# Performance work log

Hardware: AMD Instinct MI355X
Metric: run time of the kernel (lower is better)

Reference implementation:

```python
import jax, jax.numpy as jnp
import numpy as np

K = 4096   # infeatures
N = 11008  # outfeatures
T = 8192   # tokens (batch*seq)
GROUP = 32
E8M0_BIAS = 127
E2M1_VALS = jnp.array([0.0, 0.5, 1.0, 1.5, 2.0, 3.0, 4.0, 6.0], dtype=jnp.float32)


def setup_inputs() -> dict:
    key = jax.random.key(0)
    k1, k2, k3, k4 = jax.random.split(key, 4)
    x = jax.random.normal(k1, (T, K), dtype=jnp.float32)
    # packed fp4: 8 nibbles per int32 along the in-feature axis -> [K//8, N]
    weight_packed = jax.random.randint(k2, (K // 8, N), 0, 2147483647, dtype=jnp.int32)
    # e8m0 exponents near the bias so 2^(e-127) stays well-conditioned in fp32
    weight_scale_e8m0 = 112 + jax.random.randint(k3, (K // GROUP, N), 0, 30, dtype=jnp.int32)
    bias = jax.random.normal(k4, (N,), dtype=jnp.float32)
    return {"x": x, "weight_packed": weight_packed,
            "weight_scale_e8m0": weight_scale_e8m0, "bias": bias}


def dequantize_weight(weight_packed, weight_scale_e8m0):
    # unpack 8 fp4 nibbles per int32: nibble j -> in-feature row r*8 + j
    shifts = (jnp.arange(8, dtype=jnp.int32) * 4)[None, :, None]       # [1,8,1]
    nib = (weight_packed[:, None, :] >> shifts) & 0xF                   # [K//8,8,N]
    mag = E2M1_VALS[nib & 0x7]                                           # e2m1 magnitude
    sign = jnp.where((nib >> 3) & 1 == 1, -1.0, 1.0).astype(jnp.float32)
    w = (mag * sign).reshape(K, N)
    # per-group e8m0 scale: 2^(e - 127), groups of 32 along in-features
    scale = jnp.exp2((weight_scale_e8m0 - E8M0_BIAS).astype(jnp.float32))  # [K//32,N]
    w = (w.reshape(K // GROUP, GROUP, N) * scale[:, None, :]).reshape(K, N)
    return w


def reference(x, weight_packed, weight_scale_e8m0, bias):
    w = dequantize_weight(weight_packed, weight_scale_e8m0)  # [K, N]
    return x @ w + bias                                       # [T, N]
```

## Files before the change

### kernel.cpp

```cpp
#include <hip/hip_runtime.h>


#define TDIM 8192
#define KDIM 4096
#define NDIM 11008

typedef __attribute__((ext_vector_type(8))) short short8;
typedef __attribute__((ext_vector_type(8))) unsigned short ushort8;
typedef __attribute__((ext_vector_type(4))) float f32x4;

__device__ __forceinline__ unsigned short f2bf(float f) {
    unsigned int u = __float_as_uint(f);
    u += 0x7FFFu + ((u >> 16) & 1u);
    return (unsigned short)(u >> 16);
}

__device__ __forceinline__ unsigned short nib2bf(unsigned int v, int e) {
    unsigned int m3 = v & 7u;
    if (m3 == 0u) return 0;
    unsigned int s = (v & 8u) << 12;
    unsigned int E = (unsigned int)e + (m3 >> 1) - 1u;
    unsigned int man = (m3 >= 2u) ? ((m3 & 1u) << 6) : 0u;
    return (unsigned short)(s | (E << 7) | man);
}

__device__ __forceinline__ void gload_lds16(const void* g, void* l) {
    __builtin_amdgcn_global_load_lds(
        (const __attribute__((address_space(1))) void*)g,
        (__attribute__((address_space(3))) void*)l, 16, 0, 0);
}

__global__ __launch_bounds__(256) void convert_x(const float* __restrict__ x,
                                                 unsigned short* __restrict__ xbf) {
    size_t i = ((size_t)blockIdx.x * 256 + threadIdx.x) * 8;
    float4 v0 = *(const float4*)(x + i);
    float4 v1 = *(const float4*)(x + i + 4);
    ushort8 r;
    r[0] = f2bf(v0.x); r[1] = f2bf(v0.y); r[2] = f2bf(v0.z); r[3] = f2bf(v0.w);
    r[4] = f2bf(v1.x); r[5] = f2bf(v1.y); r[6] = f2bf(v1.z); r[7] = f2bf(v1.w);
    *(ushort8*)(xbf + i) = r;
}

__global__ __launch_bounds__(256) void dequant_w(const int* __restrict__ wp,
                                                 const int* __restrict__ wse,
                                                 unsigned short* __restrict__ wt) {
    __shared__ int sT[64][65];
    const int tid = threadIdx.x;
    const int n0 = blockIdx.x * 64;
    const int r0 = blockIdx.y * 64;

    #pragma unroll
    for (int i = 0; i < 16; ++i) {
        int idx = i * 256 + tid;
        int r = idx >> 6, n = idx & 63;
        sT[r][n] = wp[(size_t)(r0 + r) * NDIM + n0 + n];
    }
    __syncthreads();
    #pragma unroll
    for (int i = 0; i < 16; ++i) {
        int idx = i * 256 + tid;
        int n = idx >> 6, r = idx & 63;
        unsigned int p = (unsigned int)sT[r][n];
        int e = wse[(size_t)((r0 + r) >> 2) * NDIM + n0 + n];
        ushort8 o;
        #pragma unroll
        for (int j = 0; j < 8; ++j) o[j] = nib2bf((p >> (4 * j)) & 0xFu, e);
        *(ushort8*)(wt + (size_t)(n0 + n) * KDIM + (size_t)(r0 + r) * 8) = o;
    }
}

#define STG(PJ0, PJ1, GOFF, C, MAT, HK)                                        \
    do {                                                                       \
        gload_lds16((PJ0) + (GOFF), ldsW + (C)*32768 + (MAT)*16384 + (HK)*8192);           \
        gload_lds16((PJ1) + (GOFF), ldsW + (C)*32768 + (MAT)*16384 + (HK)*8192 + 4096);    \
    } while (0)

#define RD_A(CB, KS, MH, DST)                                                                  \
    DST[0] = *(const short8*)(ldsC + (CB)*65536 + (KS)*16384 + ((MH)*4 + 0)*1024 + aoff);      \
    DST[1] = *(const short8*)(ldsC + (CB)*65536 + (KS)*16384 + ((MH)*4 + 1)*1024 + aoff);      \
    DST[2] = *(const short8*)(ldsC + (CB)*65536 + (KS)*16384 + ((MH)*4 + 2)*1024 + aoff);      \
    DST[3] = *(const short8*)(ldsC + (CB)*65536 + (KS)*16384 + ((MH)*4 + 3)*1024 + aoff);

#define RD_B(CB, KS, DST)                                                                      \
    DST[0] = *(const short8*)(ldsC + (CB)*65536 + 32768 + (KS)*16384 + 0*1024 + boff);         \
    DST[1] = *(const short8*)(ldsC + (CB)*65536 + 32768 + (KS)*16384 + 1*1024 + boff);         \
    DST[2] = *(const short8*)(ldsC + (CB)*65536 + 32768 + (KS)*16384 + 2*1024 + boff);         \
    DST[3] = *(const short8*)(ldsC + (CB)*65536 + 32768 + (KS)*16384 + 3*1024 + boff);

#define CLUSTER(A, B, MH)                                                      \
    __builtin_amdgcn_s_setprio(1);                                             \
    _Pragma("unroll")                                                          \
    for (int i_ = 0; i_ < 4; ++i_) {                                           \
        _Pragma("unroll")                                                      \
        for (int n_ = 0; n_ < 4; ++n_)                                         \
            acc[(MH)*4 + i_][n_] = __builtin_amdgcn_mfma_f32_16x16x32_bf16(    \
                A[i_], B[n_], acc[(MH)*4 + i_][n_], 0, 0, 0);                  \
    }                                                                          \
    __builtin_amdgcn_s_setprio(0);

#define BODY(T, C)                                                             \
    do {                                                                       \
                       \
        if ((T) < 63) STG(pA0, pA1, 96, (C)^1, 0, 1);                          \
        RD_A((C), 0, 1, aY)                                                    \
        CLUSTER(aX, bX, 0)                                                     \
                \
        if ((T) < 63) STG(pB0, pB1, 96, (C)^1, 1, 1);                          \
        RD_B((C), 1, bY)                                                       \
        RD_A((C), 1, 0, aX)                                                    \
        CLUSTER(aY, bX, 1)                                                     \
        \
        if ((T) < 63) asm volatile("s_waitcnt vmcnt(4)" ::: "memory");         \
        __builtin_amdgcn_s_barrier();                                          \
               \
        if ((T) < 62) STG(pA0, pA1, 128, (C), 0, 0);                           \
        RD_A((C), 1, 1, aY)                                                    \
        CLUSTER(aX, bY, 0)                                                     \
                       \
        if ((T) < 62) STG(pB0, pB1, 128, (C), 1, 0);                           \
        if ((T) < 63) { RD_B((C)^1, 0, bX) RD_A((C)^1, 0, 0, aX) }             \
        CLUSTER(aY, bY, 1)                                                     \
            \
        if ((T) < 62)       asm volatile("s_waitcnt vmcnt(4)" ::: "memory");   \
        else if ((T) == 62) asm volatile("s_waitcnt vmcnt(0)" ::: "memory");   \
        __builtin_amdgcn_s_barrier();                                          \
        pA0 += 64; pA1 += 64; pB0 += 64; pB1 += 64;                            \
    } while (0)

__global__ __launch_bounds__(512, 1) void gemm256(const unsigned short* __restrict__ xbf,
                                                  const unsigned short* __restrict__ wt,
                                                  const float* __restrict__ bias,
                                                  float* __restrict__ out) {
    __shared__ __attribute__((aligned(16))) unsigned short lds[2][2][16384];
    const int tid = threadIdx.x;
    const int l = tid & 63, wid = tid >> 6;
    const int wm = wid >> 2, wn = wid & 3;

    int b = blockIdx.x;
    int swz = (b & 7) * 172 + (b >> 3);
    int band = swz / 344;
    int r = swz % 344;
    int st = r >> 5; if (st > 10) st = 10;
    int ii = r - (st << 5);
    int w = (st < 10) ? 4 : 3;
    const int bm0 = (band * 8 + ii / w) * 256;
    const int bn0 = (st * 4 + ii % w) * 256;

    int rs0, ks0, rs1, ks1;
    {
        int chunk = wid * 64 + l;
        int cin = chunk & 63;
        cin ^= ((cin >> 5) & 1) << 1;
        rs0 = (chunk >> 6) * 16 + (cin >> 2);
        ks0 = (cin & 3) * 8;
        chunk = 512 + wid * 64 + l;
        cin = chunk & 63;
        cin ^= ((cin >> 5) & 1) << 1;
        rs1 = (chunk >> 6) * 16 + (cin >> 2);
        ks1 = (cin & 3) * 8;
    }

    const unsigned short* pA0 = xbf + (size_t)(bm0 + rs0) * KDIM + ks0;
    const unsigned short* pA1 = xbf + (size_t)(bm0 + rs1) * KDIM + ks1;
    const unsigned short* pB0 = wt + (size_t)(bn0 + rs0) * KDIM + ks0;
    const unsigned short* pB1 = wt + (size_t)(bn0 + rs1) * KDIM + ks1;

    unsigned short* ldsW = &lds[0][0][0] + wid * 512;
    const char* ldsC = (const char*)&lds[0][0][0];

    const int lbyte = (((l & 15) * 64 + ((l >> 4) << 4))) ^ ((l & 8) << 2);
    const int aoff = wm * 8192 + lbyte;
    const int boff = wn * 4096 + lbyte;

    f32x4 acc[8][4] = {};
    short8 aX[4], aY[4], bX[4], bY[4];

    STG(pA0, pA1, 0, 0, 0, 0);
    STG(pB0, pB1, 0, 0, 1, 0);
    STG(pA0, pA1, 32, 0, 0, 1);
    STG(pB0, pB1, 32, 0, 1, 1);
    STG(pA0, pA1, 64, 1, 0, 0);
    STG(pB0, pB1, 64, 1, 1, 0);
    asm volatile("s_waitcnt vmcnt(4)" ::: "memory");
    __builtin_amdgcn_s_barrier();
    RD_B(0, 0, bX)
    RD_A(0, 0, 0, aX)

    for (int tt = 0; tt < 32; ++tt) {
        const int ta = 2 * tt;
        BODY(ta, 0);
        BODY(ta + 1, 1);
    }

    const int crow = (l >> 4) * 4, ccol = l & 15;
    #pragma unroll
    for (int nf = 0; nf < 4; ++nf) {
        int col = bn0 + wn * 64 + nf * 16 + ccol;
        float bv = bias[col];
        #pragma unroll
        for (int m = 0; m < 8; ++m) {
            int row0 = bm0 + wm * 128 + m * 16 + crow;
            #pragma unroll
            for (int j2 = 0; j2 < 4; ++j2)
                __builtin_nontemporal_store(acc[m][nf][j2] + bv,
                                            &out[(size_t)(row0 + j2) * NDIM + col]);
        }
    }
}

__global__ __launch_bounds__(256, 2) void gemm_fused(const float* __restrict__ x,
                                                     const int* __restrict__ wp,
                                                     const int* __restrict__ wse,
                                                     const float* __restrict__ bias,
                                                     float* __restrict__ out) {
    __shared__ __attribute__((aligned(16))) unsigned short lA[128 * 64];
    __shared__ __attribute__((aligned(16))) unsigned short lB[128 * 64];
    const int tid = threadIdx.x;
    const int l = tid & 63, wid = tid >> 6;
    const int bn0 = blockIdx.x * 128, bm0 = blockIdx.y * 128;
    const int wm = wid >> 1, wn = wid & 1;

    f32x4 acc[4][4] = {};

    for (int k0 = 0; k0 < KDIM; k0 += 64) {
        float4 av0[4], av1[4];
        unsigned int bp[4];
        int be[4];
        #pragma unroll
        for (int i = 0; i < 4; ++i) {
            int seg = i * 256 + tid;
            int row = seg >> 3, kseg = seg & 7;
            const float4* p = (const float4*)(x + (size_t)(bm0 + row) * KDIM + k0 + kseg * 8);
            av0[i] = p[0]; av1[i] = p[1];
        }
        #pragma unroll
        for (int i = 0; i < 4; ++i) {
            int idx = i * 256 + tid;
            int ln = idx & 127, lr = idx >> 7;
            bp[i] = ((const unsigned int*)wp)[(size_t)(k0 / 8 + lr) * NDIM + bn0 + ln];
            be[i] = wse[(size_t)((k0 + lr * 8) >> 5) * NDIM + bn0 + ln];
        }
        #pragma unroll
        for (int i = 0; i < 4; ++i) {
            int seg = i * 256 + tid;
            int row = seg >> 3, kseg = seg & 7;
            ushort8 r;
            r[0] = f2bf(av0[i].x); r[1] = f2bf(av0[i].y); r[2] = f2bf(av0[i].z); r[3] = f2bf(av0[i].w);
            r[4] = f2bf(av1[i].x); r[5] = f2bf(av1[i].y); r[6] = f2bf(av1[i].z); r[7] = f2bf(av1[i].w);
            *(ushort8*)&lA[row * 64 + kseg * 8] = r;
        }
        #pragma unroll
        for (int i = 0; i < 4; ++i) {
            int idx = i * 256 + tid;
            int ln = idx & 127, lr = idx >> 7;
            unsigned int p = bp[i];
            int e = be[i];
            ushort8 r;
            #pragma unroll
            for (int j = 0; j < 8; ++j) r[j] = nib2bf((p >> (4 * j)) & 0xFu, e);
            *(ushort8*)&lB[ln * 64 + lr * 8] = r;
        }
        __syncthreads();
        #pragma unroll
        for (int kc = 0; kc < 2; ++kc) {
            short8 a[4], bb[4];
            #pragma unroll
            for (int f = 0; f < 4; ++f) {
                a[f] = *(const short8*)&lA[(wm * 64 + f * 16 + (l & 15)) * 64 + kc * 32 + (l >> 4) * 8];
                bb[f] = *(const short8*)&lB[(wn * 64 + f * 16 + (l & 15)) * 64 + kc * 32 + (l >> 4) * 8];
            }
            #pragma unroll
            for (int fm = 0; fm < 4; ++fm)
                #pragma unroll
                for (int fn = 0; fn < 4; ++fn)
                    acc[fm][fn] = __builtin_amdgcn_mfma_f32_16x16x32_bf16(a[fm], bb[fn], acc[fm][fn], 0, 0, 0);
        }
        __syncthreads();
    }

    const int crow = (l >> 4) * 4, ccol = l & 15;
    #pragma unroll
    for (int fn = 0; fn < 4; ++fn) {
        int col = bn0 + wn * 64 + fn * 16 + ccol;
        float bv = bias[col];
        #pragma unroll
        for (int fm = 0; fm < 4; ++fm) {
            int row0 = bm0 + wm * 64 + fm * 16 + crow;
            #pragma unroll
            for (int j = 0; j < 4; ++j)
                out[(size_t)(row0 + j) * NDIM + col] = acc[fm][fn][j] + bv;
        }
    }
}

extern "C" void kernel_launch(void* const* d_in, const int* in_sizes, int n_in,
                              void* d_out, int out_size, void* d_ws, size_t ws_size,
                              hipStream_t stream) {
    (void)in_sizes; (void)n_in; (void)out_size;
    const float* x = (const float*)d_in[0];
    const int* wp = (const int*)d_in[1];
    const int* wse = (const int*)d_in[2];
    const float* bias = (const float*)d_in[3];
    float* out = (float*)d_out;

    const size_t xbf_bytes = (size_t)TDIM * KDIM * 2;
    const size_t wt_bytes = (size_t)NDIM * KDIM * 2;

    if (ws_size >= xbf_bytes + wt_bytes) {
        unsigned short* xbf = (unsigned short*)d_ws;
        unsigned short* wt = (unsigned short*)((char*)d_ws + xbf_bytes);
        hipLaunchKernelGGL(convert_x, dim3((TDIM * KDIM) / (256 * 8)), dim3(256), 0, stream, x, xbf);
        hipLaunchKernelGGL(dequant_w, dim3(NDIM / 64, (KDIM / 8) / 64), dim3(256), 0, stream, wp, wse, wt);
        hipLaunchKernelGGL(gemm256, dim3((NDIM / 256) * (TDIM / 256)), dim3(512), 0, stream, xbf, wt, bias, out);
    } else {
        hipLaunchKernelGGL(gemm_fused, dim3(NDIM / 128, TDIM / 128), dim3(256), 0, stream, x, wp, wse, bias, out);
    }
}
```

Before: 688.1 us.

## Switch main GEMM from 16x16x32 to 32x32x16 bf16 MFMA tiles

Replaces the 16x16x32 bf16 MFMA instructions in the 256-tile GEMM with 32x32x16 MFMAs. The LDS fragment read offsets, the accumulator layout (f32x16 [4][2]) and the epilogue row/column mapping are reworked to match. Larger MFMA tiles cut the instruction count and give more operand reuse per LDS read, but they change the bank access pattern of the swizzled LDS reads and have a longer per-instruction latency.

```diff
diff --git a/kernel.cpp b/kernel.cpp
--- a/kernel.cpp
+++ b/kernel.cpp
@@ -8,6 +8,7 @@
 typedef __attribute__((ext_vector_type(8))) short short8;
 typedef __attribute__((ext_vector_type(8))) unsigned short ushort8;
 typedef __attribute__((ext_vector_type(4))) float f32x4;
+typedef __attribute__((ext_vector_type(16))) float f32x16;
 
 __device__ __forceinline__ unsigned short f2bf(float f) {
     unsigned int u = __float_as_uint(f);
@@ -75,26 +76,29 @@
         gload_lds16((PJ1) + (GOFF), ldsW + (C)*32768 + (MAT)*16384 + (HK)*8192 + 4096);    \
     } while (0)
 
-#define RD_A(CB, KS, MH, DST)                                                                  \
-    DST[0] = *(const short8*)(ldsC + (CB)*65536 + (KS)*16384 + ((MH)*4 + 0)*1024 + aoff);      \
-    DST[1] = *(const short8*)(ldsC + (CB)*65536 + (KS)*16384 + ((MH)*4 + 1)*1024 + aoff);      \
-    DST[2] = *(const short8*)(ldsC + (CB)*65536 + (KS)*16384 + ((MH)*4 + 2)*1024 + aoff);      \
-    DST[3] = *(const short8*)(ldsC + (CB)*65536 + (KS)*16384 + ((MH)*4 + 3)*1024 + aoff);
-
-#define RD_B(CB, KS, DST)                                                                      \
-    DST[0] = *(const short8*)(ldsC + (CB)*65536 + 32768 + (KS)*16384 + 0*1024 + boff);         \
-    DST[1] = *(const short8*)(ldsC + (CB)*65536 + 32768 + (KS)*16384 + 1*1024 + boff);         \
-    DST[2] = *(const short8*)(ldsC + (CB)*65536 + 32768 + (KS)*16384 + 2*1024 + boff);         \
-    DST[3] = *(const short8*)(ldsC + (CB)*65536 + 32768 + (KS)*16384 + 3*1024 + boff);
-
-#define CLUSTER(A, B, MH)                                                      \
+#define RD_A32(CB, KS, MH, DST)                                                                \
+    DST[0] = *(const short8*)(ldsC + (CB)*65536 + (KS)*16384 + (((MH)*2+0)*2)*1024 + aoff + ofK0); \
+    DST[1] = *(const short8*)(ldsC + (CB)*65536 + (KS)*16384 + (((MH)*2+0)*2)*1024 + aoff + ofK1); \
+    DST[2] = *(const short8*)(ldsC + (CB)*65536 + (KS)*16384 + (((MH)*2+1)*2)*1024 + aoff + ofK0); \
+    DST[3] = *(const short8*)(ldsC + (CB)*65536 + (KS)*16384 + (((MH)*2+1)*2)*1024 + aoff + ofK1);
+
+#define RD_B32(CB, KS, DST)                                                                    \
+    DST[0] = *(const short8*)(ldsC + (CB)*65536 + 32768 + (KS)*16384 + 0*2048 + boff + ofK0);  \
+    DST[1] = *(const short8*)(ldsC + (CB)*65536 + 32768 + (KS)*16384 + 0*2048 + boff + ofK1);  \
+    DST[2] = *(const short8*)(ldsC + (CB)*65536 + 32768 + (KS)*16384 + 1*2048 + boff + ofK0);  \
+    DST[3] = *(const short8*)(ldsC + (CB)*65536 + 32768 + (KS)*16384 + 1*2048 + boff + ofK1);
+
+#define CLUSTER32(A, B, MH)                                                    \
     __builtin_amdgcn_s_setprio(1);                                             \
     _Pragma("unroll")                                                          \
-    for (int i_ = 0; i_ < 4; ++i_) {                                           \
+    for (int kk_ = 0; kk_ < 2; ++kk_) {                                        \
         _Pragma("unroll")                                                      \
-        for (int n_ = 0; n_ < 4; ++n_)                                         \
-            acc[(MH)*4 + i_][n_] = __builtin_amdgcn_mfma_f32_16x16x32_bf16(    \
-                A[i_], B[n_], acc[(MH)*4 + i_][n_], 0, 0, 0);                  \
+        for (int m_ = 0; m_ < 2; ++m_) {                                       \
+            _Pragma("unroll")                                                  \
+            for (int n_ = 0; n_ < 2; ++n_)                                     \
+                acc[(MH)*2 + m_][n_] = __builtin_amdgcn_mfma_f32_32x32x16_bf16( \
+                    A[m_*2 + kk_], B[n_*2 + kk_], acc[(MH)*2 + m_][n_], 0, 0, 0); \
+        }                                                                      \
     }                                                                          \
     __builtin_amdgcn_s_setprio(0);
 
@@ -102,25 +106,23 @@
     do {                                                                       \
                        \
         if ((T) < 63) STG(pA0, pA1, 96, (C)^1, 0, 1);                          \
-        RD_A((C), 0, 1, aY)                                                    \
-        CLUSTER(aX, bX, 0)                                                     \
+        RD_A32((C), 0, 1, aY)                                                  \
+        CLUSTER32(aX, bX, 0)                                                   \
                 \
         if ((T) < 63) STG(pB0, pB1, 96, (C)^1, 1, 1);                          \
-        RD_B((C), 1, bY)                                                       \
-        RD_A((C), 1, 0, aX)                                                    \
-        CLUSTER(aY, bX, 1)                                                     \
-        \
+        RD_B32((C), 1, bY)                                                     \
+        RD_A32((C), 1, 0, aX)                                                  \
+        CLUSTER32(aY, bX, 1)                                                   \
         if ((T) < 63) asm volatile("s_waitcnt vmcnt(4)" ::: "memory");         \
         __builtin_amdgcn_s_barrier();                                          \
-               \
+              \
         if ((T) < 62) STG(pA0, pA1, 128, (C), 0, 0);                           \
-        RD_A((C), 1, 1, aY)                                                    \
-        CLUSTER(aX, bY, 0)                                                     \
+        RD_A32((C), 1, 1, aY)                                                  \
+        CLUSTER32(aX, bY, 0)                                                   \
                        \
         if ((T) < 62) STG(pB0, pB1, 128, (C), 1, 0);                           \
-        if ((T) < 63) { RD_B((C)^1, 0, bX) RD_A((C)^1, 0, 0, aX) }             \
-        CLUSTER(aY, bY, 1)                                                     \
-            \
+        if ((T) < 63) { RD_B32((C)^1, 0, bX) RD_A32((C)^1, 0, 0, aX) }         \
+        CLUSTER32(aY, bY, 1)                                                   \
         if ((T) < 62)       asm volatile("s_waitcnt vmcnt(4)" ::: "memory");   \
         else if ((T) == 62) asm volatile("s_waitcnt vmcnt(0)" ::: "memory");   \
         __builtin_amdgcn_s_barrier();                                          \
@@ -168,11 +170,14 @@
     unsigned short* ldsW = &lds[0][0][0] + wid * 512;
     const char* ldsC = (const char*)&lds[0][0][0];
 
-    const int lbyte = (((l & 15) * 64 + ((l >> 4) << 4))) ^ ((l & 8) << 2);
-    const int aoff = wm * 8192 + lbyte;
-    const int boff = wn * 4096 + lbyte;
-
-    f32x4 acc[8][4] = {};
+    const int s3 = (l >> 3) & 1;
+    const int lbase = ((l >> 4) & 1) * 1024 + (l & 15) * 64 + ((l >> 5) << 4);
+    const int ofK0 = lbase + (s3 << 5);
+    const int ofK1 = lbase + ((s3 ^ 1) << 5);
+    const int aoff = wm * 8192;
+    const int boff = wn * 4096;
+
+    f32x16 acc[4][2] = {};
     short8 aX[4], aY[4], bX[4], bY[4];
 
     STG(pA0, pA1, 0, 0, 0, 0);
@@ -183,27 +188,28 @@
     STG(pB0, pB1, 64, 1, 1, 0);
     asm volatile("s_waitcnt vmcnt(4)" ::: "memory");
     __builtin_amdgcn_s_barrier();
-    RD_B(0, 0, bX)
-    RD_A(0, 0, 0, aX)
+    RD_B32(0, 0, bX)
+    RD_A32(0, 0, 0, aX)
 
     for (int tt = 0; tt < 32; ++tt) {
-        const int ta = 2 * tt;
-        BODY(ta, 0);
-        BODY(ta + 1, 1);
-    }
-
-    const int crow = (l >> 4) * 4, ccol = l & 15;
+        BODY(2 * tt, 0);
+        BODY(2 * tt + 1, 1);
+    }
+
+    const int ecol = l & 31, erow = (l >> 5) * 4;
     #pragma unroll
-    for (int nf = 0; nf < 4; ++nf) {
-        int col = bn0 + wn * 64 + nf * 16 + ccol;
+    for (int nb = 0; nb < 2; ++nb) {
+        int col = bn0 + wn * 64 + nb * 32 + ecol;
         float bv = bias[col];
         #pragma unroll
-        for (int m = 0; m < 8; ++m) {
-            int row0 = bm0 + wm * 128 + m * 16 + crow;
-            #pragma unroll
-            for (int j2 = 0; j2 < 4; ++j2)
-                __builtin_nontemporal_store(acc[m][nf][j2] + bv,
-                                            &out[(size_t)(row0 + j2) * NDIM + col]);
+        for (int mb = 0; mb < 4; ++mb) {
+            int rowbase = bm0 + wm * 128 + mb * 32 + erow;
+            #pragma unroll
+            for (int reg = 0; reg < 16; ++reg) {
+                int row = rowbase + (reg & 3) + 8 * (reg >> 2);
+                __builtin_nontemporal_store(acc[mb][nb][reg] + bv,
+                                            &out[(size_t)row * NDIM + col]);
+            }
         }
     }
 }
```

Result: slower. 734.8 us (+6.8%).

## Merge prepass kernels and split GEMM tail into 256x128 tiles

Applied to the files above, without the earlier changes.

Fuses the x-to-bf16 conversion and the weight dequant into one prepass launch to save a kernel launch and the gap between them. The GEMM is split in two launches: 1280 full 256x256 tiles, then the last 96 tiles processed as 192 half-width 256x128 tiles via a templated NF=2 variant. The split is meant to balance the final wave across CUs, since 1376 tiles do not divide evenly over the compute units. In exchange it adds an extra launch, and the half-width tiles have lower arithmetic intensity.

```diff
diff --git a/kernel.cpp b/kernel.cpp
--- a/kernel.cpp
+++ b/kernel.cpp
@@ -30,24 +30,26 @@
         (__attribute__((address_space(3))) void*)l, 16, 0, 0);
 }
 
-__global__ __launch_bounds__(256) void convert_x(const float* __restrict__ x,
-                                                 unsigned short* __restrict__ xbf) {
-    size_t i = ((size_t)blockIdx.x * 256 + threadIdx.x) * 8;
-    float4 v0 = *(const float4*)(x + i);
-    float4 v1 = *(const float4*)(x + i + 4);
-    ushort8 r;
-    r[0] = f2bf(v0.x); r[1] = f2bf(v0.y); r[2] = f2bf(v0.z); r[3] = f2bf(v0.w);
-    r[4] = f2bf(v1.x); r[5] = f2bf(v1.y); r[6] = f2bf(v1.z); r[7] = f2bf(v1.w);
-    *(ushort8*)(xbf + i) = r;
-}
-
-__global__ __launch_bounds__(256) void dequant_w(const int* __restrict__ wp,
-                                                 const int* __restrict__ wse,
-                                                 unsigned short* __restrict__ wt) {
+__global__ __launch_bounds__(256) void prepass(const float* __restrict__ x,
+                                               unsigned short* __restrict__ xbf,
+                                               const int* __restrict__ wp,
+                                               const int* __restrict__ wse,
+                                               unsigned short* __restrict__ wt) {
     __shared__ int sT[64][65];
     const int tid = threadIdx.x;
-    const int n0 = blockIdx.x * 64;
-    const int r0 = blockIdx.y * 64;
+    if (blockIdx.x < 16384) {
+        size_t i = ((size_t)blockIdx.x * 256 + tid) * 8;
+        float4 v0 = *(const float4*)(x + i);
+        float4 v1 = *(const float4*)(x + i + 4);
+        ushort8 r;
+        r[0] = f2bf(v0.x); r[1] = f2bf(v0.y); r[2] = f2bf(v0.z); r[3] = f2bf(v0.w);
+        r[4] = f2bf(v1.x); r[5] = f2bf(v1.y); r[6] = f2bf(v1.z); r[7] = f2bf(v1.w);
+        *(ushort8*)(xbf + i) = r;
+        return;
+    }
+    const int bb = blockIdx.x - 16384;
+    const int n0 = (bb % 172) * 64;
+    const int r0 = (bb / 172) * 64;
 
     #pragma unroll
     for (int i = 0; i < 16; ++i) {
@@ -69,64 +71,77 @@
     }
 }
 
-#define STG(PJ0, PJ1, GOFF, C, MAT, HK)                                        \
-    do {                                                                       \
-        gload_lds16((PJ0) + (GOFF), ldsW + (C)*32768 + (MAT)*16384 + (HK)*8192);           \
-        gload_lds16((PJ1) + (GOFF), ldsW + (C)*32768 + (MAT)*16384 + (HK)*8192 + 4096);    \
+#define STG_A(GOFF, C, HK)                                                                  \
+    do {                                                                                    \
+        gload_lds16(pA0 + (GOFF), ldsW + (C)*32768 + (HK)*8192);                            \
+        gload_lds16(pA1 + (GOFF), ldsW + (C)*32768 + (HK)*8192 + 4096);                     \
     } while (0)
 
-#define RD_A(CB, KS, MH, DST)                                                                  \
-    DST[0] = *(const short8*)(ldsC + (CB)*65536 + (KS)*16384 + ((MH)*4 + 0)*1024 + aoff);      \
-    DST[1] = *(const short8*)(ldsC + (CB)*65536 + (KS)*16384 + ((MH)*4 + 1)*1024 + aoff);      \
-    DST[2] = *(const short8*)(ldsC + (CB)*65536 + (KS)*16384 + ((MH)*4 + 2)*1024 + aoff);      \
+#define STG_B(GOFF, C, HK)                                                                  \
+    do {                                                                                    \
+        gload_lds16(pB0 + (GOFF), ldsW + (C)*32768 + 16384 + (HK)*8192);                    \
+        if constexpr (NF == 4)                                                              \
+            gload_lds16(pB1 + (GOFF), ldsW + (C)*32768 + 16384 + (HK)*8192 + 4096);         \
+    } while (0)
+
+#define RD_A(CB, KS, MH, DST)                                                                      \
+    DST[0] = *(const short8*)(ldsC + (CB)*65536 + (KS)*16384 + ((MH)*4 + 0)*1024 + aoff);          \
+    DST[1] = *(const short8*)(ldsC + (CB)*65536 + (KS)*16384 + ((MH)*4 + 1)*1024 + aoff);          \
+    DST[2] = *(const short8*)(ldsC + (CB)*65536 + (KS)*16384 + ((MH)*4 + 2)*1024 + aoff);          \
     DST[3] = *(const short8*)(ldsC + (CB)*65536 + (KS)*16384 + ((MH)*4 + 3)*1024 + aoff);
 
-#define RD_B(CB, KS, DST)                                                                      \
-    DST[0] = *(const short8*)(ldsC + (CB)*65536 + 32768 + (KS)*16384 + 0*1024 + boff);         \
-    DST[1] = *(const short8*)(ldsC + (CB)*65536 + 32768 + (KS)*16384 + 1*1024 + boff);         \
-    DST[2] = *(const short8*)(ldsC + (CB)*65536 + 32768 + (KS)*16384 + 2*1024 + boff);         \
-    DST[3] = *(const short8*)(ldsC + (CB)*65536 + 32768 + (KS)*16384 + 3*1024 + boff);
+#define RD_B(CB, KS, DST)                                                                          \
+    DST[0] = *(const short8*)(ldsC + (CB)*65536 + 32768 + (KS)*16384 + 0*1024 + boff);             \
+    DST[1] = *(const short8*)(ldsC + (CB)*65536 + 32768 + (KS)*16384 + 1*1024 + boff);             \
+    if constexpr (NF == 4) {                                                                       \
+        DST[2] = *(const short8*)(ldsC + (CB)*65536 + 32768 + (KS)*16384 + 2*1024 + boff);         \
+        DST[3] = *(const short8*)(ldsC + (CB)*65536 + 32768 + (KS)*16384 + 3*1024 + boff);         \
+    }
 
 #define CLUSTER(A, B, MH)                                                      \
     __builtin_amdgcn_s_setprio(1);                                             \
     _Pragma("unroll")                                                          \
     for (int i_ = 0; i_ < 4; ++i_) {                                           \
         _Pragma("unroll")                                                      \
-        for (int n_ = 0; n_ < 4; ++n_)                                         \
+        for (int n_ = 0; n_ < NF; ++n_)                                        \
             acc[(MH)*4 + i_][n_] = __builtin_amdgcn_mfma_f32_16x16x32_bf16(    \
                 A[i_], B[n_], acc[(MH)*4 + i_][n_], 0, 0, 0);                  \
     }                                                                          \
     __builtin_amdgcn_s_setprio(0);
 
+#define VWAIT_STEADY()                                                         \
+    do { if constexpr (NF == 4) asm volatile("s_waitcnt vmcnt(4)" ::: "memory"); \
+         else                   asm volatile("s_waitcnt vmcnt(3)" ::: "memory"); } while (0)
+
 #define BODY(T, C)                                                             \
     do {                                                                       \
                        \
-        if ((T) < 63) STG(pA0, pA1, 96, (C)^1, 0, 1);                          \
+        if ((T) < 63) STG_A(96, (C)^1, 1);                                     \
         RD_A((C), 0, 1, aY)                                                    \
         CLUSTER(aX, bX, 0)                                                     \
                 \
-        if ((T) < 63) STG(pB0, pB1, 96, (C)^1, 1, 1);                          \
+        if ((T) < 63) STG_B(96, (C)^1, 1);                                     \
         RD_B((C), 1, bY)                                                       \
         RD_A((C), 1, 0, aX)                                                    \
         CLUSTER(aY, bX, 1)                                                     \
-        \
-        if ((T) < 63) asm volatile("s_waitcnt vmcnt(4)" ::: "memory");         \
+             \
+        if ((T) < 63) VWAIT_STEADY();                                          \
         __builtin_amdgcn_s_barrier();                                          \
-               \
-        if ((T) < 62) STG(pA0, pA1, 128, (C), 0, 0);                           \
+              \
+        if ((T) < 62) STG_A(128, (C), 0);                                      \
         RD_A((C), 1, 1, aY)                                                    \
         CLUSTER(aX, bY, 0)                                                     \
                        \
-        if ((T) < 62) STG(pB0, pB1, 128, (C), 1, 0);                           \
+        if ((T) < 62) STG_B(128, (C), 0);                                      \
         if ((T) < 63) { RD_B((C)^1, 0, bX) RD_A((C)^1, 0, 0, aX) }             \
         CLUSTER(aY, bY, 1)                                                     \
-            \
-        if ((T) < 62)       asm volatile("s_waitcnt vmcnt(4)" ::: "memory");   \
+        if ((T) < 62)       VWAIT_STEADY();                                    \
         else if ((T) == 62) asm volatile("s_waitcnt vmcnt(0)" ::: "memory");   \
         __builtin_amdgcn_s_barrier();                                          \
         pA0 += 64; pA1 += 64; pB0 += 64; pB1 += 64;                            \
     } while (0)
 
+template<int NF>
 __global__ __launch_bounds__(512, 1) void gemm256(const unsigned short* __restrict__ xbf,
                                                   const unsigned short* __restrict__ wt,
                                                   const float* __restrict__ bias,
@@ -137,14 +152,21 @@
     const int wm = wid >> 2, wn = wid & 3;
 
     int b = blockIdx.x;
-    int swz = (b & 7) * 172 + (b >> 3);
+    int swz, half = 0;
+    if constexpr (NF == 4) {
+        swz = (b & 7) * 160 + (b >> 3);
+    } else {
+        int js = (b & 7) * 24 + (b >> 3);
+        swz = 1280 + (js >> 1);
+        half = js & 1;
+    }
     int band = swz / 344;
     int r = swz % 344;
     int st = r >> 5; if (st > 10) st = 10;
     int ii = r - (st << 5);
     int w = (st < 10) ? 4 : 3;
     const int bm0 = (band * 8 + ii / w) * 256;
-    const int bn0 = (st * 4 + ii % w) * 256;
+    const int bn0 = (st * 4 + ii % w) * 256 + half * 128;
 
     int rs0, ks0, rs1, ks1;
     {
@@ -170,32 +192,29 @@
 
     const int lbyte = (((l & 15) * 64 + ((l >> 4) << 4))) ^ ((l & 8) << 2);
     const int aoff = wm * 8192 + lbyte;
-    const int boff = wn * 4096 + lbyte;
+    const int boff = wn * (NF * 1024) + lbyte;
 
     f32x4 acc[8][4] = {};
     short8 aX[4], aY[4], bX[4], bY[4];
 
-    STG(pA0, pA1, 0, 0, 0, 0);
-    STG(pB0, pB1, 0, 0, 1, 0);
-    STG(pA0, pA1, 32, 0, 0, 1);
-    STG(pB0, pB1, 32, 0, 1, 1);
-    STG(pA0, pA1, 64, 1, 0, 0);
-    STG(pB0, pB1, 64, 1, 1, 0);
-    asm volatile("s_waitcnt vmcnt(4)" ::: "memory");
+    STG_A(0, 0, 0);   STG_B(0, 0, 0);
+    STG_A(32, 0, 1);  STG_B(32, 0, 1);
+    STG_A(64, 1, 0);  STG_B(64, 1, 0);
+    if constexpr (NF == 4) asm volatile("s_waitcnt vmcnt(4)" ::: "memory");
+    else                   asm volatile("s_waitcnt vmcnt(3)" ::: "memory");
     __builtin_amdgcn_s_barrier();
     RD_B(0, 0, bX)
     RD_A(0, 0, 0, aX)
 
     for (int tt = 0; tt < 32; ++tt) {
-        const int ta = 2 * tt;
-        BODY(ta, 0);
-        BODY(ta + 1, 1);
+        BODY(2 * tt, 0);
+        BODY(2 * tt + 1, 1);
     }
 
     const int crow = (l >> 4) * 4, ccol = l & 15;
     #pragma unroll
-    for (int nf = 0; nf < 4; ++nf) {
-        int col = bn0 + wn * 64 + nf * 16 + ccol;
+    for (int nf = 0; nf < NF; ++nf) {
+        int col = bn0 + wn * (NF * 16) + nf * 16 + ccol;
         float bv = bias[col];
         #pragma unroll
         for (int m = 0; m < 8; ++m) {
@@ -309,9 +328,9 @@
     if (ws_size >= xbf_bytes + wt_bytes) {
         unsigned short* xbf = (unsigned short*)d_ws;
         unsigned short* wt = (unsigned short*)((char*)d_ws + xbf_bytes);
-        hipLaunchKernelGGL(convert_x, dim3((TDIM * KDIM) / (256 * 8)), dim3(256), 0, stream, x, xbf);
-        hipLaunchKernelGGL(dequant_w, dim3(NDIM / 64, (KDIM / 8) / 64), dim3(256), 0, stream, wp, wse, wt);
-        hipLaunchKernelGGL(gemm256, dim3((NDIM / 256) * (TDIM / 256)), dim3(512), 0, stream, xbf, wt, bias, out);
+        prepass<<<dim3(16384 + 1376), dim3(256), 0, stream>>>(x, xbf, wp, wse, wt);
+        gemm256<4><<<dim3(1280), dim3(512), 0, stream>>>(xbf, wt, bias, out);
+        gemm256<2><<<dim3(192), dim3(512), 0, stream>>>(xbf, wt, bias, out);
     } else {
         hipLaunchKernelGGL(gemm_fused, dim3(NDIM / 128, TDIM / 128), dim3(256), 0, stream, x, wp, wse, bias, out);
     }
```

Result: faster. 673.9 us (-2.1%).
